# Kernel tuning notes

Measured on AMD Instinct MI355X. Metric: run time of the kernel, lower is better.

The kernel has to match this reference:

```python
import jax, jax.numpy as jnp
import numpy as np

EMBED = 1024
HEADS = 16
INTERNAL = 1024  # embedding_dim // downsample_rate
HEAD_DIM = INTERNAL // HEADS


def setup_inputs() -> dict:
    key = jax.random.key(0)
    ks = jax.random.split(key, 12)
    B, S = 2, 2048
    s_in = 1.0 / np.sqrt(EMBED)
    s_out = 1.0 / np.sqrt(INTERNAL)
    return {
        "queries": jax.random.normal(ks[0], (B, S, EMBED), jnp.float32),
        "keys": jax.random.normal(ks[1], (B, S, EMBED), jnp.float32),
        "values": jax.random.normal(ks[2], (B, S, EMBED), jnp.float32),
        "Wq": jax.random.uniform(ks[3], (EMBED, INTERNAL), jnp.float32, -s_in, s_in),
        "bq": jax.random.uniform(ks[4], (INTERNAL,), jnp.float32, -s_in, s_in),
        "Wk": jax.random.uniform(ks[5], (EMBED, INTERNAL), jnp.float32, -s_in, s_in),
        "bk": jax.random.uniform(ks[6], (INTERNAL,), jnp.float32, -s_in, s_in),
        "Wv": jax.random.uniform(ks[7], (EMBED, INTERNAL), jnp.float32, -s_in, s_in),
        "bv": jax.random.uniform(ks[8], (INTERNAL,), jnp.float32, -s_in, s_in),
        "Wo": jax.random.uniform(ks[9], (INTERNAL, EMBED), jnp.float32, -s_out, s_out),
        "bo": jax.random.uniform(ks[10], (EMBED,), jnp.float32, -s_out, s_out),
    }


def _split_heads(x):
    B, S, D = x.shape
    return x.reshape(B, S, HEADS, D // HEADS).transpose(0, 2, 1, 3)  # bhsd


def reference(queries, keys, values, Wq, bq, Wk, bk, Wv, bv, Wo, bo):
    q = _split_heads(queries @ Wq + bq)
    k = _split_heads(keys @ Wk + bk)
    v = _split_heads(values @ Wv + bv)
    # NOTE: original scales by 1/sqrt(internal_dim), not 1/sqrt(head_dim)
    scale = 1.0 / np.sqrt(INTERNAL).astype(np.float32)
    scores = jnp.einsum("bhqd,bhkd->bhqk", q, k) * scale
    probs = jax.nn.softmax(scores, axis=-1)
    out = jnp.einsum("bhqk,bhkd->bhqd", probs, v)
    B, H, S, Dh = out.shape
    out = out.transpose(0, 2, 1, 3).reshape(B, S, H * Dh)
    return out @ Wo + bo
```

## Files before the change

### kernel.cpp

```cpp
#include <hip/hip_runtime.h>
#include <stdint.h>

typedef unsigned short u16;
typedef __attribute__((ext_vector_type(8))) short short8;
typedef __attribute__((ext_vector_type(4))) float f32x4;
typedef __attribute__((ext_vector_type(8))) unsigned short u16x8;
typedef __attribute__((ext_vector_type(4))) unsigned short u16x4;

#if __has_builtin(__builtin_amdgcn_exp2f)
#define EXP2(x) __builtin_amdgcn_exp2f(x)
#else
#define EXP2(x) exp2f(x)
#endif

__device__ __forceinline__ u16 f2bf(float f) {
  union { float f; uint32_t u; } v; v.f = f;
  uint32_t r = (v.u + 0x7FFFu + ((v.u >> 16) & 1u)) >> 16;
  return (u16)r;
}

__device__ __forceinline__ void gload_lds16(const void* g, void* l) {
  __builtin_amdgcn_global_load_lds(
      (const __attribute__((address_space(1))) void*)g,
      (__attribute__((address_space(3))) void*)l,
      16, 0, 0);
}

__global__ __launch_bounds__(256) void cvt_x(const float* __restrict__ q,
                                             const float* __restrict__ k,
                                             const float* __restrict__ v,
                                             u16* __restrict__ dst) {
  const float* src = blockIdx.z == 0 ? q : (blockIdx.z == 1 ? k : v);
  u16* d = dst + (size_t)blockIdx.z * (4096u * 1024u);
  size_t i = ((size_t)blockIdx.x * 256 + threadIdx.x) * 8;
  float4 a = *(const float4*)(src + i);
  float4 b = *(const float4*)(src + i + 4);
  u16x8 o;
  o[0] = f2bf(a.x); o[1] = f2bf(a.y); o[2] = f2bf(a.z); o[3] = f2bf(a.w);
  o[4] = f2bf(b.x); o[5] = f2bf(b.y); o[6] = f2bf(b.z); o[7] = f2bf(b.w);
  *(u16x8*)(d + i) = o;
}

__global__ __launch_bounds__(256) void cvt_wt(const float* __restrict__ Wq,
                                              const float* __restrict__ Wk,
                                              const float* __restrict__ Wv,
                                              const float* __restrict__ Wo,
                                              u16* __restrict__ Wt4) {
  const float* W = blockIdx.z == 0 ? Wq : (blockIdx.z == 1 ? Wk
                   : (blockIdx.z == 2 ? Wv : Wo));
  u16* Wt = Wt4 + (size_t)blockIdx.z * (1024u * 1024u);
  __shared__ u16 tile[64][65];
  int kt = blockIdx.x * 64, nt = blockIdx.y * 64;
  int t = threadIdx.x;
#pragma unroll
  for (int r = 0; r < 4; ++r) {
    int id = t + r * 256;
    int kk = id >> 4, c4 = id & 15;
    float4 vv = *(const float4*)(W + (size_t)(kt + kk) * 1024 + nt + c4 * 4);
    tile[kk][c4 * 4 + 0] = f2bf(vv.x);
    tile[kk][c4 * 4 + 1] = f2bf(vv.y);
    tile[kk][c4 * 4 + 2] = f2bf(vv.z);
    tile[kk][c4 * 4 + 3] = f2bf(vv.w);
  }
  __syncthreads();
#pragma unroll
  for (int r = 0; r < 4; ++r) {
    int id = t + r * 256;
    int n = id >> 4, kc = id & 15;
    u16x4 o;
    o[0] = tile[kc * 4 + 0][n];
    o[1] = tile[kc * 4 + 1][n];
    o[2] = tile[kc * 4 + 2][n];
    o[3] = tile[kc * 4 + 3][n];
    *(u16x4*)(Wt + (size_t)(nt + n) * 1024 + kt + kc * 4) = o;
  }
}

template <bool F32OUT>
__device__ __forceinline__ void gemm_tile(const u16* __restrict__ A,
                                          const u16* __restrict__ Bt,
                                          const float* __restrict__ bias,
                                          u16* __restrict__ Cb,
                                          float* __restrict__ Cf,
                                          float scale, int bm, int bn) {
  __shared__ u16 Alds[128 * 64];
  __shared__ u16 Blds[128 * 64];
  const int tid = threadIdx.x;
  const int lane = tid & 63, w = tid >> 6;
  const int wm = (w >> 1) * 64, wn = (w & 1) * 64;
  const int l15 = lane & 15, lg = lane >> 4;

  f32x4 acc[4][4] = {};

  int srow[4], scol[4], soff[4];
#pragma unroll
  for (int i = 0; i < 4; ++i) {
    int o = (w * 4 + i) * 1024 + lane * 16;
    int row = o >> 7;
    int kc = ((o >> 4) & 7) ^ (row & 7);
    srow[i] = row; scol[i] = kc * 8; soff[i] = o;
  }

  for (int kt = 0; kt < 16; ++kt) {
    __syncthreads();
#pragma unroll
    for (int i = 0; i < 4; ++i) {
      gload_lds16(A + (size_t)(bm * 128 + srow[i]) * 1024 + kt * 64 + scol[i],
                  (char*)Alds + soff[i]);
      gload_lds16(Bt + (size_t)(bn * 128 + srow[i]) * 1024 + kt * 64 + scol[i],
                  (char*)Blds + soff[i]);
    }
    __syncthreads();
#pragma unroll
    for (int ks = 0; ks < 2; ++ks) {
      short8 af[4], bf[4];
#pragma unroll
      for (int m = 0; m < 4; ++m) {
        int r = wm + m * 16 + l15;
        int byt = r * 128 + ((ks * 64 + lg * 16) ^ ((r & 7) << 4));
        af[m] = *(const short8*)((const char*)Alds + byt);
      }
#pragma unroll
      for (int n = 0; n < 4; ++n) {
        int r = wn + n * 16 + l15;
        int byt = r * 128 + ((ks * 64 + lg * 16) ^ ((r & 7) << 4));
        bf[n] = *(const short8*)((const char*)Blds + byt);
      }
#pragma unroll
      for (int m = 0; m < 4; ++m)
#pragma unroll
        for (int n = 0; n < 4; ++n)
          acc[m][n] = __builtin_amdgcn_mfma_f32_16x16x32_bf16(
              af[m], bf[n], acc[m][n], 0, 0, 0);
    }
  }
#pragma unroll
  for (int m = 0; m < 4; ++m) {
    int row0 = bm * 128 + wm + m * 16 + lg * 4;
#pragma unroll
    for (int n = 0; n < 4; ++n) {
      int col = bn * 128 + wn + n * 16 + l15;
      float bvv = bias[col];
#pragma unroll
      for (int r = 0; r < 4; ++r) {
        float v = (acc[m][n][r] + bvv) * scale;
        if (F32OUT)
          Cf[(size_t)(row0 + r) * 1024 + col] = v;
        else
          Cb[(size_t)(row0 + r) * 1024 + col] = f2bf(v);
      }
    }
  }
}

__global__ __launch_bounds__(256) void proj_kernel(const u16* __restrict__ X3,
                                                   const u16* __restrict__ Wt3,
                                                   const float* __restrict__ bq,
                                                   const float* __restrict__ bk,
                                                   const float* __restrict__ bv,
                                                   u16* __restrict__ out3) {
  int z = blockIdx.z;
  const float* bias = z == 0 ? bq : (z == 1 ? bk : bv);
  float scale = z == 0 ? 0.045084220f : 1.0f;
  gemm_tile<false>(X3 + (size_t)z * 4096 * 1024, Wt3 + (size_t)z * 1024 * 1024,
                   bias, out3 + (size_t)z * 4096 * 1024, nullptr, scale,
                   blockIdx.x, blockIdx.y);
}

__global__ __launch_bounds__(256) void outproj_kernel(const u16* __restrict__ Att,
                                                      const u16* __restrict__ Wot,
                                                      const float* __restrict__ bo,
                                                      float* __restrict__ out) {
  gemm_tile<true>(Att, Wot, bo, nullptr, out, 1.0f, blockIdx.x, blockIdx.y);
}

__global__ __launch_bounds__(256) void vt_kernel(const u16* __restrict__ v,
                                                 u16* __restrict__ vt) {
  int bh = blockIdx.y;
  int sbase = blockIdx.x * 64;
  int b = bh >> 4, h = bh & 15;
  __shared__ u16 tile[64][65];
  int t = threadIdx.x;
#pragma unroll
  for (int r = 0; r < 2; ++r) {
    int id = t + r * 256;
    int s = id >> 3, dc = id & 7;
    u16x8 x = *(const u16x8*)(v + (size_t)(b * 2048 + sbase + s) * 1024 +
                              h * 64 + dc * 8);
#pragma unroll
    for (int j = 0; j < 8; ++j) tile[s][dc * 8 + j] = x[j];
  }
  __syncthreads();
#pragma unroll
  for (int r = 0; r < 2; ++r) {
    int id = t + r * 256;
    int d = id >> 3, sc = id & 7;
    u16x8 o;
#pragma unroll
    for (int j = 0; j < 8; ++j) o[j] = tile[sc * 8 + j][d];
    *(u16x8*)(vt + ((size_t)bh * 64 + d) * 2048 + sbase + sc * 8) = o;
  }
}

__global__ __launch_bounds__(256) void attn_kernel(const u16* __restrict__ q,
                                                   const u16* __restrict__ k,
                                                   const u16* __restrict__ vt,
                                                   u16* __restrict__ att) {
  __shared__ u16 Klds[64 * 64];
  __shared__ u16 Vlds[64 * 64];
  __shared__ u16 Plds[4][16 * 64];
  const int tid = threadIdx.x, lane = tid & 63, w = tid >> 6;
  const int l15 = lane & 15, lg = lane >> 4;
  const int bh = blockIdx.y, b = bh >> 4, h = bh & 15;
  const int qbase = blockIdx.x * 64 + w * 16;

  short8 aq[2];
#pragma unroll
  for (int ks = 0; ks < 2; ++ks)
    aq[ks] = *(const short8*)(q + (size_t)(b * 2048 + qbase + l15) * 1024 +
                              h * 64 + ks * 32 + lg * 8);

  float lsum[4] = {0.f, 0.f, 0.f, 0.f};
  f32x4 o_acc[4] = {};

  const int o1 = w * 2048 + lane * 16;
  u16* pw = Plds[w];

  for (int t = 0; t < 32; ++t) {
    const int kbase = t * 64;
    __syncthreads();
#pragma unroll
    for (int i = 0; i < 2; ++i) {
      int o = o1 + i * 1024;
      int row = o >> 7;
      int kc = ((o >> 4) & 7) ^ (row & 7);
      gload_lds16(k + (size_t)(b * 2048 + kbase + row) * 1024 + h * 64 + kc * 8,
                  (char*)Klds + o);
      gload_lds16(vt + ((size_t)bh * 64 + row) * 2048 + kbase + kc * 8,
                  (char*)Vlds + o);
    }
    __syncthreads();

    f32x4 s[4];
#pragma unroll
    for (int n = 0; n < 4; ++n) {
      f32x4 c = {};
#pragma unroll
      for (int ks = 0; ks < 2; ++ks) {
        int rr = n * 16 + l15;
        int byt = rr * 128 + ((ks * 64 + lg * 16) ^ ((rr & 7) << 4));
        short8 bk_ = *(const short8*)((const char*)Klds + byt);
        c = __builtin_amdgcn_mfma_f32_16x16x32_bf16(aq[ks], bk_, c, 0, 0, 0);
      }
      s[n] = c;
    }

#pragma unroll
    for (int n = 0; n < 4; ++n) {
#pragma unroll
      for (int r = 0; r < 4; ++r) {
        float p = EXP2(s[n][r]);
        uint32_t u = __float_as_uint(p);
        int qrow = lg * 4 + r, key = n * 16 + l15;
        int byt = qrow * 128 + ((key * 2) ^ ((qrow & 7) << 4));
        *(u16*)((char*)pw + byt) = (u16)(u >> 16);
        lsum[r] += __uint_as_float(u & 0xffff0000u);
      }
    }
    asm volatile("s_waitcnt lgkmcnt(0)" ::: "memory");

#pragma unroll
    for (int ks = 0; ks < 2; ++ks) {
      int abyt = l15 * 128 + ((ks * 64 + lg * 16) ^ ((l15 & 7) << 4));
      short8 ap = *(const short8*)((const char*)pw + abyt);
#pragma unroll
      for (int n = 0; n < 4; ++n) {
        int rr = n * 16 + l15;
        int vbyt = rr * 128 + ((ks * 64 + lg * 16) ^ ((rr & 7) << 4));
        short8 bv_ = *(const short8*)((const char*)Vlds + vbyt);
        o_acc[n] = __builtin_amdgcn_mfma_f32_16x16x32_bf16(ap, bv_, o_acc[n],
                                                           0, 0, 0);
      }
    }
  }

  float rinv[4];
#pragma unroll
  for (int r = 0; r < 4; ++r) {
    float l = lsum[r];
    l += __shfl_xor(l, 1);
    l += __shfl_xor(l, 2);
    l += __shfl_xor(l, 4);
    l += __shfl_xor(l, 8);
    rinv[r] = 1.0f / l;
  }
#pragma unroll
  for (int n = 0; n < 4; ++n)
#pragma unroll
    for (int r = 0; r < 4; ++r) {
      float vv = o_acc[n][r] * rinv[r];
      att[(size_t)(b * 2048 + qbase + lg * 4 + r) * 1024 + h * 64 + n * 16 +
          l15] = f2bf(vv);
    }
}

extern "C" void kernel_launch(void* const* d_in, const int* in_sizes, int n_in,
                              void* d_out, int out_size, void* d_ws,
                              size_t ws_size, hipStream_t stream) {
  const float* Q  = (const float*)d_in[0];
  const float* K  = (const float*)d_in[1];
  const float* V  = (const float*)d_in[2];
  const float* Wq = (const float*)d_in[3];
  const float* bq = (const float*)d_in[4];
  const float* Wk = (const float*)d_in[5];
  const float* bk = (const float*)d_in[6];
  const float* Wv = (const float*)d_in[7];
  const float* bv = (const float*)d_in[8];
  const float* Wo = (const float*)d_in[9];
  const float* bo = (const float*)d_in[10];
  float* out = (float*)d_out;

  u16* ws = (u16*)d_ws;
  const size_t SZX = (size_t)4096 * 1024;
  const size_t SZW = (size_t)1024 * 1024;
  u16* Xbf   = ws;
  u16* Wtbf  = ws + 3 * SZX;
  u16* QKVbf = Wtbf + 4 * SZW;
  u16* VTbf  = QKVbf + 3 * SZX;
  u16* ATTbf = VTbf + SZX;

  hipLaunchKernelGGL(cvt_x, dim3(2048, 1, 3), dim3(256), 0, stream, Q, K, V,
                     Xbf);
  hipLaunchKernelGGL(cvt_wt, dim3(16, 16, 4), dim3(256), 0, stream, Wq, Wk, Wv,
                     Wo, Wtbf);
  hipLaunchKernelGGL(proj_kernel, dim3(32, 8, 3), dim3(256), 0, stream, Xbf,
                     Wtbf, bq, bk, bv, QKVbf);
  hipLaunchKernelGGL(vt_kernel, dim3(32, 32), dim3(256), 0, stream,
                     QKVbf + 2 * SZX, VTbf);
  hipLaunchKernelGGL(attn_kernel, dim3(32, 32), dim3(256), 0, stream, QKVbf,
                     QKVbf + SZX, VTbf, ATTbf);
  hipLaunchKernelGGL(outproj_kernel, dim3(32, 8), dim3(256), 0, stream, ATTbf,
                     Wtbf + 3 * SZW, bo, out);
}
```

Measured before the change: 143.5 us.

## Rewrite attention kernel with 32x32x16 MFMA, register-resident P and two-wave blocks

The attention kernel now uses 128-thread blocks, with each wave handling 32 query rows through 32x32x16 bf16 MFMAs instead of 16x16x32. Scores are computed transposed (K as A operand), and the probabilities are packed to bf16 and exchanged across half-waves with shuffles. This keeps P in registers and removes the LDS round trip for P and its wait. The output is staged through LDS so global stores are coalesced 16-byte writes. The cost is fewer threads per block to load the K/V tiles, more registers per lane, and truncating rather than rounding on the final bf16 conversion.

```diff
diff --git a/kernel.cpp b/kernel.cpp
--- a/kernel.cpp
+++ b/kernel.cpp
@@ -4,8 +4,10 @@
 typedef unsigned short u16;
 typedef __attribute__((ext_vector_type(8))) short short8;
 typedef __attribute__((ext_vector_type(4))) float f32x4;
+typedef __attribute__((ext_vector_type(16))) float f32x16;
 typedef __attribute__((ext_vector_type(8))) unsigned short u16x8;
 typedef __attribute__((ext_vector_type(4))) unsigned short u16x4;
+typedef __attribute__((ext_vector_type(4))) uint32_t u32x4;
 
 #if __has_builtin(__builtin_amdgcn_exp2f)
 #define EXP2(x) __builtin_amdgcn_exp2f(x)
@@ -17,6 +19,10 @@
   union { float f; uint32_t u; } v; v.f = f;
   uint32_t r = (v.u + 0x7FFFu + ((v.u >> 16) & 1u)) >> 16;
   return (u16)r;
+}
+
+__device__ __forceinline__ uint32_t pack2(float a, float b) {
+  return (__float_as_uint(b) & 0xffff0000u) | (__float_as_uint(a) >> 16);
 }
 
 __device__ __forceinline__ void gload_lds16(const void* g, void* l) {
@@ -202,106 +208,119 @@
   }
 }
 
-__global__ __launch_bounds__(256) void attn_kernel(const u16* __restrict__ q,
+__global__ __launch_bounds__(128) void attn_kernel(const u16* __restrict__ q,
                                                    const u16* __restrict__ k,
                                                    const u16* __restrict__ vt,
                                                    u16* __restrict__ att) {
-  __shared__ u16 Klds[64 * 64];
-  __shared__ u16 Vlds[64 * 64];
-  __shared__ u16 Plds[4][16 * 64];
+  __shared__ u16 smem[8192];
   const int tid = threadIdx.x, lane = tid & 63, w = tid >> 6;
-  const int l15 = lane & 15, lg = lane >> 4;
+  const int l31 = lane & 31, hi = lane >> 5;
   const int bh = blockIdx.y, b = bh >> 4, h = bh & 15;
-  const int qbase = blockIdx.x * 64 + w * 16;
-
-  short8 aq[2];
-#pragma unroll
-  for (int ks = 0; ks < 2; ++ks)
-    aq[ks] = *(const short8*)(q + (size_t)(b * 2048 + qbase + l15) * 1024 +
-                              h * 64 + ks * 32 + lg * 8);
-
-  float lsum[4] = {0.f, 0.f, 0.f, 0.f};
-  f32x4 o_acc[4] = {};
-
-  const int o1 = w * 2048 + lane * 16;
-  u16* pw = Plds[w];
+  const int qb = blockIdx.x * 64 + w * 32;
+
+  short8 qf[4];
+  const u16* qrow = q + (size_t)(b * 2048 + qb + l31) * 1024 + h * 64 + hi * 8;
+#pragma unroll
+  for (int s = 0; s < 4; ++s) qf[s] = *(const short8*)(qrow + s * 16);
+
+  f32x16 acc0 = {}, acc1 = {};
+  float lsum = 0.f;
+
+  int srow[4], scol[4], soff[4];
+#pragma unroll
+  for (int i = 0; i < 4; ++i) {
+    int o = w * 4096 + i * 1024 + lane * 16;
+    int row = o >> 7;
+    int kc = ((o >> 4) & 7) ^ (row & 7);
+    srow[i] = row; scol[i] = kc * 8; soff[i] = o;
+  }
+  const u16* ksrc = k + (size_t)b * 2048 * 1024 + h * 64;
+  const u16* vsrc = vt + (size_t)bh * 64 * 2048;
+  const char* KL = (const char*)smem;
+  const char* VL = (const char*)smem + 8192;
 
   for (int t = 0; t < 32; ++t) {
     const int kbase = t * 64;
     __syncthreads();
 #pragma unroll
-    for (int i = 0; i < 2; ++i) {
-      int o = o1 + i * 1024;
-      int row = o >> 7;
-      int kc = ((o >> 4) & 7) ^ (row & 7);
-      gload_lds16(k + (size_t)(b * 2048 + kbase + row) * 1024 + h * 64 + kc * 8,
-                  (char*)Klds + o);
-      gload_lds16(vt + ((size_t)bh * 64 + row) * 2048 + kbase + kc * 8,
-                  (char*)Vlds + o);
+    for (int i = 0; i < 4; ++i) {
+      gload_lds16(ksrc + (size_t)(kbase + srow[i]) * 1024 + scol[i],
+                  (char*)smem + soff[i]);
+      gload_lds16(vsrc + (size_t)srow[i] * 2048 + kbase + scol[i],
+                  (char*)smem + 8192 + soff[i]);
     }
     __syncthreads();
 
-    f32x4 s[4];
-#pragma unroll
-    for (int n = 0; n < 4; ++n) {
-      f32x4 c = {};
-#pragma unroll
-      for (int ks = 0; ks < 2; ++ks) {
-        int rr = n * 16 + l15;
-        int byt = rr * 128 + ((ks * 64 + lg * 16) ^ ((rr & 7) << 4));
-        short8 bk_ = *(const short8*)((const char*)Klds + byt);
-        c = __builtin_amdgcn_mfma_f32_16x16x32_bf16(aq[ks], bk_, c, 0, 0, 0);
-      }
-      s[n] = c;
-    }
-
-#pragma unroll
-    for (int n = 0; n < 4; ++n) {
-#pragma unroll
-      for (int r = 0; r < 4; ++r) {
-        float p = EXP2(s[n][r]);
-        uint32_t u = __float_as_uint(p);
-        int qrow = lg * 4 + r, key = n * 16 + l15;
-        int byt = qrow * 128 + ((key * 2) ^ ((qrow & 7) << 4));
-        *(u16*)((char*)pw + byt) = (u16)(u >> 16);
-        lsum[r] += __uint_as_float(u & 0xffff0000u);
-      }
-    }
-    asm volatile("s_waitcnt lgkmcnt(0)" ::: "memory");
-
-#pragma unroll
-    for (int ks = 0; ks < 2; ++ks) {
-      int abyt = l15 * 128 + ((ks * 64 + lg * 16) ^ ((l15 & 7) << 4));
-      short8 ap = *(const short8*)((const char*)pw + abyt);
-#pragma unroll
-      for (int n = 0; n < 4; ++n) {
-        int rr = n * 16 + l15;
-        int vbyt = rr * 128 + ((ks * 64 + lg * 16) ^ ((rr & 7) << 4));
-        short8 bv_ = *(const short8*)((const char*)Vlds + vbyt);
-        o_acc[n] = __builtin_amdgcn_mfma_f32_16x16x32_bf16(ap, bv_, o_acc[n],
-                                                           0, 0, 0);
-      }
-    }
-  }
-
-  float rinv[4];
-#pragma unroll
-  for (int r = 0; r < 4; ++r) {
-    float l = lsum[r];
-    l += __shfl_xor(l, 1);
-    l += __shfl_xor(l, 2);
-    l += __shfl_xor(l, 4);
-    l += __shfl_xor(l, 8);
-    rinv[r] = 1.0f / l;
-  }
-#pragma unroll
-  for (int n = 0; n < 4; ++n)
-#pragma unroll
-    for (int r = 0; r < 4; ++r) {
-      float vv = o_acc[n][r] * rinv[r];
-      att[(size_t)(b * 2048 + qbase + lg * 4 + r) * 1024 + h * 64 + n * 16 +
-          l15] = f2bf(vv);
-    }
+#pragma unroll
+    for (int kg = 0; kg < 2; ++kg) {
+      f32x16 sc = {};
+#pragma unroll
+      for (int s = 0; s < 4; ++s) {
+        int row = kg * 32 + l31;
+        int byt = row * 128 + ((s * 32 + hi * 16) ^ ((row & 7) << 4));
+        short8 ak = *(const short8*)(KL + byt);
+        sc = __builtin_amdgcn_mfma_f32_32x32x16_bf16(ak, qf[s], sc, 0, 0, 0);
+      }
+      uint32_t pw_[4][2];
+#pragma unroll
+      for (int g = 0; g < 4; ++g) {
+        float p0 = EXP2(sc[4 * g + 0]);
+        float p1 = EXP2(sc[4 * g + 1]);
+        float p2 = EXP2(sc[4 * g + 2]);
+        float p3 = EXP2(sc[4 * g + 3]);
+        lsum += (p0 + p1) + (p2 + p3);
+        pw_[g][0] = pack2(p0, p1);
+        pw_[g][1] = pack2(p2, p3);
+      }
+#pragma unroll
+      for (int c = 0; c < 2; ++c) {
+        uint32_t s0 = hi ? pw_[2 * c][0] : pw_[2 * c + 1][0];
+        uint32_t s1 = hi ? pw_[2 * c][1] : pw_[2 * c + 1][1];
+        uint32_t r0 = (uint32_t)__shfl_xor((int)s0, 32);
+        uint32_t r1 = (uint32_t)__shfl_xor((int)s1, 32);
+        u32x4 fw;
+        fw[0] = hi ? r0 : pw_[2 * c][0];
+        fw[1] = hi ? r1 : pw_[2 * c][1];
+        fw[2] = hi ? pw_[2 * c + 1][0] : r0;
+        fw[3] = hi ? pw_[2 * c + 1][1] : r1;
+        short8 pf = __builtin_bit_cast(short8, fw);
+        int colv = kg * 64 + c * 32 + hi * 16;
+        {
+          int row = l31;
+          int byt = row * 128 + (colv ^ ((row & 7) << 4));
+          short8 bv_ = *(const short8*)(VL + byt);
+          acc0 = __builtin_amdgcn_mfma_f32_32x32x16_bf16(pf, bv_, acc0, 0, 0, 0);
+        }
+        {
+          int row = 32 + l31;
+          int byt = row * 128 + (colv ^ ((row & 7) << 4));
+          short8 bv_ = *(const short8*)(VL + byt);
+          acc1 = __builtin_amdgcn_mfma_f32_32x32x16_bf16(pf, bv_, acc1, 0, 0, 0);
+        }
+      }
+    }
+  }
+
+  float ltot = lsum + __shfl_xor(lsum, 32);
+  float rinv = 1.0f / ltot;
+  __syncthreads();
+  u16* tw = smem + w * 2048;
+#pragma unroll
+  for (int r = 0; r < 16; ++r) {
+    int row = (r & 3) + 8 * (r >> 2) + 4 * hi;
+    float ri = __shfl(rinv, row);
+    tw[row * 64 + l31] = (u16)(__float_as_uint(acc0[r] * ri) >> 16);
+    tw[row * 64 + 32 + l31] = (u16)(__float_as_uint(acc1[r] * ri) >> 16);
+  }
+  asm volatile("s_waitcnt lgkmcnt(0)" ::: "memory");
+  u16* abase = att + (size_t)(b * 2048 + qb) * 1024 + h * 64;
+#pragma unroll
+  for (int i = 0; i < 4; ++i) {
+    int id = lane + i * 64;
+    int row = id >> 3, ch = id & 7;
+    u16x8 vv = *(const u16x8*)(tw + row * 64 + ch * 8);
+    *(u16x8*)(abase + (size_t)row * 1024 + ch * 8) = vv;
+  }
 }
 
 extern "C" void kernel_launch(void* const* d_in, const int* in_sizes, int n_in,
@@ -337,7 +356,7 @@
                      Wtbf, bq, bk, bv, QKVbf);
   hipLaunchKernelGGL(vt_kernel, dim3(32, 32), dim3(256), 0, stream,
                      QKVbf + 2 * SZX, VTbf);
-  hipLaunchKernelGGL(attn_kernel, dim3(32, 32), dim3(256), 0, stream, QKVbf,
+  hipLaunchKernelGGL(attn_kernel, dim3(32, 32), dim3(128), 0, stream, QKVbf,
                      QKVbf + SZX, VTbf, ATTbf);
   hipLaunchKernelGGL(outproj_kernel, dim3(32, 8), dim3(256), 0, stream, ATTbf,
                      Wtbf + 3 * SZW, bo, out);
```

Measured after the change: 147.2 us. +2.6%, slower.
